# Performance work log

Hardware: AMD Instinct MI355X
Metric: run time of the kernel (lower is better)

The kernel has to match this reference:

```python
import jax, jax.numpy as jnp
import numpy as np

SCALE = float(1.0 / np.sqrt(128.0))  # 1/sqrt(q_head_dim)
NEG_BIG = -1e30


def setup_inputs() -> dict:
    key = jax.random.key(0)
    k0, k1, k2, k3, k4 = jax.random.split(key, 5)
    R, B, H, KVH, D, DV, P = 8, 8, 32, 8, 128, 128, 2048  # page_size = 1
    q = jax.random.normal(k0, (B, H, D), jnp.float32)
    k_cache = jax.random.normal(k1, (R, P, 1, KVH, D), jnp.float32)
    v_cache = jax.random.normal(k2, (R, P, 1, KVH, DV), jnp.float32)
    # each rank's shard length per batch element (>=128 so no empty shards)
    global_kv_lens = jax.random.randint(k3, (R, B), 128, P + 1, jnp.int32)
    # paged block table: page ids into that rank's cache
    block_table = jax.random.randint(k4, (R, B, P), 0, P, jnp.int32)
    return {"q": q, "k_cache": k_cache, "v_cache": v_cache,
            "global_kv_lens": global_kv_lens, "block_table": block_table}


def reference(q, k_cache, v_cache, global_kv_lens, block_table):
    R, P, page, KVH, D = k_cache.shape
    B, H, _ = q.shape
    DV = v_cache.shape[-1]
    G = H // KVH            # GQA group size
    N = P * page            # tokens per rank shard
    ridx = jnp.arange(R)[:, None, None]
    # paged KV gather per rank/batch: [R,B,N,KVH,D]
    Kg = k_cache[ridx, block_table].reshape(R, B, N, KVH, D)
    Vg = v_cache[ridx, block_table].reshape(R, B, N, KVH, DV)
    qg = q.reshape(B, KVH, G, D)
    # intra-rank split-KV attention scores: [R,B,KVH,G,N]
    s = jnp.einsum('bkgd,rbnkd->rbkgn', qg, Kg) * SCALE
    valid = (jnp.arange(N)[None, None, :] < global_kv_lens[:, :, None])
    s = jnp.where(valid[:, :, None, None, :], s, NEG_BIG)
    lse = jax.nn.logsumexp(s, axis=-1)             # per-rank softmax stats [R,B,KVH,G]
    p = jax.nn.softmax(s, axis=-1)
    out_r = jnp.einsum('rbkgn,rbnkd->rbkgd', p, Vg)  # per-rank partial output
    # inter-rank combine (online softmax across rank shards)
    m = jax.nn.logsumexp(lse, axis=0)              # [B,KVH,G]
    w = jnp.exp(lse - m)[..., None]                # [R,B,KVH,G,1]
    final = jnp.sum(w * out_r, axis=0)             # [B,KVH,G,DV]
    return final.reshape(B, H, DV)
```

## Files before the change

kernel.cpp:

```cpp
#include <hip/hip_runtime.h>
#include <hip/hip_bf16.h>
#include <math.h>

#define NR 8
#define NB 8
#define NH 32
#define NKVH 8
#define NG 4
#define ND 128
#define NDV 128
#define NDH 64
#define NPAGE 2048
#define KSTR (NKVH*ND)
#define NCH 8
#define CHUNK 256
#define NPART (NR*NCH)
#define PSTRIDE (NB*NKVH*NG)
#define QSCALE 0.088388347648318447f

typedef __attribute__((ext_vector_type(8))) short bf16x8;
typedef __attribute__((ext_vector_type(4))) float f32x4;

static __device__ __forceinline__ short f2bf(float x) {
  __hip_bfloat16 h = __float2bfloat16(x);
  return __builtin_bit_cast(short, h);
}

static __device__ __forceinline__ void gload_lds16(const float* g, float* l) {
  __builtin_amdgcn_global_load_lds(
      (__attribute__((address_space(1))) void*)g,
      (__attribute__((address_space(3))) void*)l, 16, 0, 0);
}

__global__ __launch_bounds__(256) void build_counts(
    const int* __restrict__ kv_lens, const int* __restrict__ bt_all,
    float* __restrict__ cntf) {
  const int rb = blockIdx.x;
  __shared__ int h[NPAGE];
  for (int i = threadIdx.x; i < NPAGE; i += 256) h[i] = 0;
  __syncthreads();
  const int len = kv_lens[rb];
  const int* bt = bt_all + (size_t)rb * NPAGE;
  for (int i = threadIdx.x; i < len; i += 256) atomicAdd(&h[bt[i]], 1);
  __syncthreads();
  float* o = cntf + (size_t)rb * NPAGE;
  for (int i = threadIdx.x; i < NPAGE; i += 256) o[i] = (float)h[i];
}

__global__ __launch_bounds__(256, 1) void attn_partial(
    const float* __restrict__ q,
    const float* __restrict__ k_cache,
    const float* __restrict__ v_cache,
    const float* __restrict__ cntf,
    float* __restrict__ ws_out,
    float* __restrict__ ws_lse)
{
  const int bid   = blockIdx.x;
  const int r     = bid & 7;
  const int kvh   = (bid >> 3) & 7;
  const int dh    = (bid >> 6) & 1;
  const int chunk = bid >> 7;

  const int tid  = threadIdx.x;
  const int wid  = tid >> 6;
  const int lane = tid & 63;
  const int col  = lane & 15;
  const int hq   = lane >> 4;

  __shared__ float LB[10240];

  bf16x8 qf[2][4];
#pragma unroll
  for (int gp = 0; gp < 2; ++gp) {
    const int b = col & 7;
    const int g = gp * 2 + (col >> 3);
    const float* qp = q + ((size_t)b * NH + kvh * NG + g) * ND + hq * 8;
#pragma unroll
    for (int st = 0; st < 4; ++st) {
      const float4 t0 = *(const float4*)(qp + st * 32);
      const float4 t1 = *(const float4*)(qp + st * 32 + 4);
      bf16x8 f;
      f[0] = f2bf(t0.x * QSCALE); f[1] = f2bf(t0.y * QSCALE);
      f[2] = f2bf(t0.z * QSCALE); f[3] = f2bf(t0.w * QSCALE);
      f[4] = f2bf(t1.x * QSCALE); f[5] = f2bf(t1.y * QSCALE);
      f[6] = f2bf(t1.z * QSCALE); f[7] = f2bf(t1.w * QSCALE);
      qf[gp][st] = f;
    }
  }

  const int pg0w = chunk * CHUNK + wid * 64;
  const float* Kb = k_cache + (size_t)r * NPAGE * KSTR + kvh * ND;
  const float* Vb = v_cache + (size_t)r * NPAGE * KSTR + kvh * NDV + dh * NDH;

#define STAGE_V(bf, pgt)                                                     \
  {                                                                          \
    _Pragma("unroll")                                                        \
    for (int i = 0; i < 4; ++i) {                                            \
      const float* s_ =                                                      \
          Vb + (size_t)((pgt) + 4 * i + (lane >> 4)) * KSTR + (lane & 15) * 4; \
      gload_lds16(s_, &LB[wid * 2048 + (bf) * 1024 + i * 256]);              \
    }                                                                        \
  }
#define KLOAD(dst, pgt)                                                      \
  {                                                                          \
    const float* kp_ = Kb + (size_t)((pgt) + col) * KSTR + hq * 8;           \
    _Pragma("unroll")                                                        \
    for (int st = 0; st < 4; ++st) {                                         \
      dst[2 * st]     = *(const float4*)(kp_ + st * 32);                     \
      dst[2 * st + 1] = *(const float4*)(kp_ + st * 32 + 4);                 \
    }                                                                        \
  }
#define CWLOAD(dst, pgt)                                                     \
  {                                                                          \
    _Pragma("unroll")                                                        \
    for (int rg = 0; rg < 4; ++rg)                                           \
      dst[rg] = cntf[((size_t)(r * NB + ((hq * 4 + rg) & 7))) * NPAGE +      \
                     (pgt) + col];                                           \
  }

  float4 kr[2][8];
  float  cwl[2][4];

  STAGE_V(0, pg0w);
  KLOAD(kr[0], pg0w);
  CWLOAD(cwl[0], pg0w);

  float l[2][4] = {{0.f, 0.f, 0.f, 0.f}, {0.f, 0.f, 0.f, 0.f}};
  f32x4 O[2][4];
#pragma unroll
  for (int gp = 0; gp < 2; ++gp)
#pragma unroll
    for (int rg = 0; rg < 4; ++rg) O[gp][rg] = (f32x4){0.f, 0.f, 0.f, 0.f};

#pragma unroll
  for (int t = 0; t < 4; ++t) {
    const int pgt = pg0w + t * 16;
    const int bf  = t & 1;

    if (t < 3) {
      STAGE_V(bf ^ 1, pgt + 16);
      KLOAD(kr[(t + 1) & 1], pgt + 16);
      CWLOAD(cwl[(t + 1) & 1], pgt + 16);
      asm volatile("s_waitcnt vmcnt(16)" ::: "memory");
    } else {
      asm volatile("s_waitcnt vmcnt(0)" ::: "memory");
    }

    f32x4 acc0 = (f32x4){0.f, 0.f, 0.f, 0.f};
    f32x4 acc1 = (f32x4){0.f, 0.f, 0.f, 0.f};
#pragma unroll
    for (int st = 0; st < 4; ++st) {
      const float4 a0 = kr[bf][2 * st];
      const float4 a1 = kr[bf][2 * st + 1];
      bf16x8 kf;
      kf[0] = f2bf(a0.x); kf[1] = f2bf(a0.y); kf[2] = f2bf(a0.z); kf[3] = f2bf(a0.w);
      kf[4] = f2bf(a1.x); kf[5] = f2bf(a1.y); kf[6] = f2bf(a1.z); kf[7] = f2bf(a1.w);
      acc0 = __builtin_amdgcn_mfma_f32_16x16x32_bf16(qf[0][st], kf, acc0, 0, 0, 0);
      acc1 = __builtin_amdgcn_mfma_f32_16x16x32_bf16(qf[1][st], kf, acc1, 0, 0, 0);
    }

    float p0[4], p1[4];
#pragma unroll
    for (int rg = 0; rg < 4; ++rg) {
      p0[rg] = cwl[bf][rg] * __expf(acc0[rg]);
      p1[rg] = cwl[bf][rg] * __expf(acc1[rg]);
      l[0][rg] += p0[rg];
      l[1][rg] += p1[rg];
    }
    *(f32x4*)&LB[8192 + wid * 512 + 0 * 256 + col * 16 + hq * 4] =
        (f32x4){p0[0], p0[1], p0[2], p0[3]};
    *(f32x4*)&LB[8192 + wid * 512 + 1 * 256 + col * 16 + hq * 4] =
        (f32x4){p1[0], p1[1], p1[2], p1[3]};

#pragma unroll 4
    for (int pg = 0; pg < 16; ++pg) {
      const f32x4 pw0 = *(const f32x4*)&LB[8192 + wid * 512 + pg * 16 + hq * 4];
      const f32x4 pw1 = *(const f32x4*)&LB[8192 + wid * 512 + 256 + pg * 16 + hq * 4];
      const f32x4 va  = *(const f32x4*)&LB[wid * 2048 + bf * 1024 + pg * 64 + col * 4];
#pragma unroll
      for (int rg = 0; rg < 4; ++rg) {
        O[0][rg] += pw0[rg] * va;
        O[1][rg] += pw1[rg] * va;
      }
    }
  }

#pragma unroll
  for (int mk = 1; mk <= 8; mk <<= 1)
#pragma unroll
    for (int gp = 0; gp < 2; ++gp)
#pragma unroll
      for (int rg = 0; rg < 4; ++rg) l[gp][rg] += __shfl_xor(l[gp][rg], mk);

  __syncthreads();
  if (col == 0) {
#pragma unroll
    for (int gp = 0; gp < 2; ++gp)
#pragma unroll
      for (int rg = 0; rg < 4; ++rg)
        LB[8704 + wid * 32 + gp * 16 + hq * 4 + rg] = l[gp][rg];
  }
#pragma unroll
  for (int gp = 0; gp < 2; ++gp)
#pragma unroll
    for (int rg = 0; rg < 4; ++rg) {
      const int row = (wid * 2 + gp) * 16 + hq * 4 + rg;
      *(f32x4*)&LB[row * 68 + col * 4] = O[gp][rg];
    }
  __syncthreads();

  const int row = tid >> 3;
  const int db  = tid & 7;
  const int gpo = row >> 4;
  const int qr  = row & 15;
  float L = 0.f;
#pragma unroll
  for (int w = 0; w < 4; ++w) L += LB[8704 + w * 32 + gpo * 16 + qr];
  const float inv = (L > 0.f) ? 1.f / L : 0.f;

  const int pi = r * NCH + chunk;
  const int b  = qr & 7;
  const int g  = gpo * 2 + (qr >> 3);
  const size_t prow = (((size_t)pi * NB + b) * NKVH + kvh) * NG + g;
  float* orow = ws_out + prow * NDV + dh * NDH + db * 8;
#pragma unroll
  for (int x = 0; x < 2; ++x) {
    float4 o = make_float4(0.f, 0.f, 0.f, 0.f);
#pragma unroll
    for (int w = 0; w < 4; ++w) {
      const float* s4 = &LB[((w * 2 + gpo) * 16 + qr) * 68 + db * 8 + x * 4];
      o.x += s4[0]; o.y += s4[1]; o.z += s4[2]; o.w += s4[3];
    }
    o.x *= inv; o.y *= inv; o.z *= inv; o.w *= inv;
    *(float4*)(orow + x * 4) = o;
  }
  if (db == 0) ws_lse[prow] = (L > 0.f) ? __logf(L) : -1e30f;
}

__global__ __launch_bounds__(128) void attn_combine(
    const float* __restrict__ ws_out,
    const float* __restrict__ ws_lse,
    float* __restrict__ out)
{
  const int bkg = blockIdx.x;
  const int d   = threadIdx.x;

  float mg = -INFINITY;
#pragma unroll 16
  for (int p = 0; p < NPART; ++p)
    mg = fmaxf(mg, ws_lse[p * PSTRIDE + bkg]);

  float denom = 0.f, acc = 0.f;
#pragma unroll 8
  for (int p = 0; p < NPART; ++p) {
    const float e = __expf(ws_lse[p * PSTRIDE + bkg] - mg);
    denom += e;
    acc += e * ws_out[((size_t)p * PSTRIDE + bkg) * NDV + d];
  }
  out[(size_t)bkg * NDV + d] = acc / denom;
}

extern "C" void kernel_launch(void* const* d_in, const int* in_sizes, int n_in,
                              void* d_out, int out_size, void* d_ws, size_t ws_size,
                              hipStream_t stream) {
  const float* q        = (const float*)d_in[0];
  const float* k_cache  = (const float*)d_in[1];
  const float* v_cache  = (const float*)d_in[2];
  const int*   kv_lens  = (const int*)d_in[3];
  const int*   bt       = (const int*)d_in[4];
  float* out = (float*)d_out;

  float* ws_out = (float*)d_ws;
  float* ws_lse = ws_out + (size_t)NPART * PSTRIDE * NDV;
  float* cntf   = ws_lse + NPART * PSTRIDE;

  build_counts<<<NR * NB, 256, 0, stream>>>(kv_lens, bt, cntf);
  attn_partial<<<NR * NKVH * 2 * NCH, 256, 0, stream>>>(
      q, k_cache, v_cache, cntf, ws_out, ws_lse);
  attn_combine<<<NB * NKVH * NG, NDV, 0, stream>>>(ws_out, ws_lse, out);
}
```

Measured before the change: 57.79 us.

## Merge the two V-half blocks so each block covers the full value dimension

Each attention block now handles all 128 value dimensions instead of splitting them into two halves across separate blocks. The grid is halved, which removes the duplicate K loads, QK MFMA work and exp computation that both halves used to perform. In exchange each block stages twice as much V into LDS (larger shared buffer), keeps twice as many output accumulators in registers, and adjusts the waitcnt for the extra loads. Fewer blocks (512 instead of 1024) may also reduce parallelism and latency hiding.

```diff
diff --git a/kernel.cpp b/kernel.cpp
--- a/kernel.cpp
+++ b/kernel.cpp
@@ -9,7 +9,6 @@
 #define NG 4
 #define ND 128
 #define NDV 128
-#define NDH 64
 #define NPAGE 2048
 #define KSTR (NKVH*ND)
 #define NCH 8
@@ -58,8 +57,7 @@
   const int bid   = blockIdx.x;
   const int r     = bid & 7;
   const int kvh   = (bid >> 3) & 7;
-  const int dh    = (bid >> 6) & 1;
-  const int chunk = bid >> 7;
+  const int chunk = bid >> 6;
 
   const int tid  = threadIdx.x;
   const int wid  = tid >> 6;
@@ -67,7 +65,7 @@
   const int col  = lane & 15;
   const int hq   = lane >> 4;
 
-  __shared__ float LB[10240];
+  __shared__ float LB[18432];
 
   bf16x8 qf[2][4];
 #pragma unroll
@@ -90,15 +88,15 @@
 
   const int pg0w = chunk * CHUNK + wid * 64;
   const float* Kb = k_cache + (size_t)r * NPAGE * KSTR + kvh * ND;
-  const float* Vb = v_cache + (size_t)r * NPAGE * KSTR + kvh * NDV + dh * NDH;
+  const float* Vb = v_cache + (size_t)r * NPAGE * KSTR + kvh * NDV;
 
 #define STAGE_V(bf, pgt)                                                     \
   {                                                                          \
     _Pragma("unroll")                                                        \
-    for (int i = 0; i < 4; ++i) {                                            \
+    for (int i = 0; i < 8; ++i) {                                            \
       const float* s_ =                                                      \
-          Vb + (size_t)((pgt) + 4 * i + (lane >> 4)) * KSTR + (lane & 15) * 4; \
-      gload_lds16(s_, &LB[wid * 2048 + (bf) * 1024 + i * 256]);              \
+          Vb + (size_t)((pgt) + 2 * i + (lane >> 5)) * KSTR + (lane & 31) * 4; \
+      gload_lds16(s_, &LB[wid * 4096 + (bf) * 2048 + i * 256]);              \
     }                                                                        \
   }
 #define KLOAD(dst, pgt)                                                      \
@@ -126,11 +124,14 @@
   CWLOAD(cwl[0], pg0w);
 
   float l[2][4] = {{0.f, 0.f, 0.f, 0.f}, {0.f, 0.f, 0.f, 0.f}};
-  f32x4 O[2][4];
+  f32x4 O[2][4][2];
 #pragma unroll
   for (int gp = 0; gp < 2; ++gp)
 #pragma unroll
-    for (int rg = 0; rg < 4; ++rg) O[gp][rg] = (f32x4){0.f, 0.f, 0.f, 0.f};
+    for (int rg = 0; rg < 4; ++rg) {
+      O[gp][rg][0] = (f32x4){0.f, 0.f, 0.f, 0.f};
+      O[gp][rg][1] = (f32x4){0.f, 0.f, 0.f, 0.f};
+    }
 
 #pragma unroll
   for (int t = 0; t < 4; ++t) {
@@ -141,7 +142,7 @@
       STAGE_V(bf ^ 1, pgt + 16);
       KLOAD(kr[(t + 1) & 1], pgt + 16);
       CWLOAD(cwl[(t + 1) & 1], pgt + 16);
-      asm volatile("s_waitcnt vmcnt(16)" ::: "memory");
+      asm volatile("s_waitcnt vmcnt(20)" ::: "memory");
     } else {
       asm volatile("s_waitcnt vmcnt(0)" ::: "memory");
     }
@@ -167,20 +168,24 @@
       l[0][rg] += p0[rg];
       l[1][rg] += p1[rg];
     }
-    *(f32x4*)&LB[8192 + wid * 512 + 0 * 256 + col * 16 + hq * 4] =
+    *(f32x4*)&LB[16384 + wid * 512 + 0 * 256 + col * 16 + hq * 4] =
         (f32x4){p0[0], p0[1], p0[2], p0[3]};
-    *(f32x4*)&LB[8192 + wid * 512 + 1 * 256 + col * 16 + hq * 4] =
+    *(f32x4*)&LB[16384 + wid * 512 + 1 * 256 + col * 16 + hq * 4] =
         (f32x4){p1[0], p1[1], p1[2], p1[3]};
 
 #pragma unroll 4
     for (int pg = 0; pg < 16; ++pg) {
-      const f32x4 pw0 = *(const f32x4*)&LB[8192 + wid * 512 + pg * 16 + hq * 4];
-      const f32x4 pw1 = *(const f32x4*)&LB[8192 + wid * 512 + 256 + pg * 16 + hq * 4];
-      const f32x4 va  = *(const f32x4*)&LB[wid * 2048 + bf * 1024 + pg * 64 + col * 4];
+      const f32x4 pw0 = *(const f32x4*)&LB[16384 + wid * 512 + pg * 16 + hq * 4];
+      const f32x4 pw1 = *(const f32x4*)&LB[16384 + wid * 512 + 256 + pg * 16 + hq * 4];
+      const float* vl = &LB[wid * 4096 + bf * 2048 + pg * 128 + col * 4];
+      const f32x4 va = *(const f32x4*)vl;
+      const f32x4 vb2 = *(const f32x4*)(vl + 64);
 #pragma unroll
       for (int rg = 0; rg < 4; ++rg) {
-        O[0][rg] += pw0[rg] * va;
-        O[1][rg] += pw1[rg] * va;
+        O[0][rg][0] += pw0[rg] * va;
+        O[0][rg][1] += pw0[rg] * vb2;
+        O[1][rg][0] += pw1[rg] * va;
+        O[1][rg][1] += pw1[rg] * vb2;
       }
     }
   }
@@ -198,14 +203,15 @@
     for (int gp = 0; gp < 2; ++gp)
 #pragma unroll
       for (int rg = 0; rg < 4; ++rg)
-        LB[8704 + wid * 32 + gp * 16 + hq * 4 + rg] = l[gp][rg];
+        LB[16896 + (wid * 2 + gp) * 16 + hq * 4 + rg] = l[gp][rg];
   }
 #pragma unroll
   for (int gp = 0; gp < 2; ++gp)
 #pragma unroll
     for (int rg = 0; rg < 4; ++rg) {
       const int row = (wid * 2 + gp) * 16 + hq * 4 + rg;
-      *(f32x4*)&LB[row * 68 + col * 4] = O[gp][rg];
+      *(f32x4*)&LB[row * 132 + col * 4]      = O[gp][rg][0];
+      *(f32x4*)&LB[row * 132 + 64 + col * 4] = O[gp][rg][1];
     }
   __syncthreads();
 
@@ -215,20 +221,20 @@
   const int qr  = row & 15;
   float L = 0.f;
 #pragma unroll
-  for (int w = 0; w < 4; ++w) L += LB[8704 + w * 32 + gpo * 16 + qr];
+  for (int w = 0; w < 4; ++w) L += LB[16896 + (w * 2 + gpo) * 16 + qr];
   const float inv = (L > 0.f) ? 1.f / L : 0.f;
 
   const int pi = r * NCH + chunk;
   const int b  = qr & 7;
   const int g  = gpo * 2 + (qr >> 3);
   const size_t prow = (((size_t)pi * NB + b) * NKVH + kvh) * NG + g;
-  float* orow = ws_out + prow * NDV + dh * NDH + db * 8;
-#pragma unroll
-  for (int x = 0; x < 2; ++x) {
+  float* orow = ws_out + prow * NDV + db * 16;
+#pragma unroll
+  for (int x = 0; x < 4; ++x) {
     float4 o = make_float4(0.f, 0.f, 0.f, 0.f);
 #pragma unroll
     for (int w = 0; w < 4; ++w) {
-      const float* s4 = &LB[((w * 2 + gpo) * 16 + qr) * 68 + db * 8 + x * 4];
+      const float* s4 = &LB[((w * 2 + gpo) * 16 + qr) * 132 + db * 16 + x * 4];
       o.x += s4[0]; o.y += s4[1]; o.z += s4[2]; o.w += s4[3];
     }
     o.x *= inv; o.y *= inv; o.z *= inv; o.w *= inv;
@@ -275,7 +281,7 @@
   float* cntf   = ws_lse + NPART * PSTRIDE;
 
   build_counts<<<NR * NB, 256, 0, stream>>>(kv_lens, bt, cntf);
-  attn_partial<<<NR * NKVH * 2 * NCH, 256, 0, stream>>>(
+  attn_partial<<<NR * NKVH * NCH, 256, 0, stream>>>(
       q, k_cache, v_cache, cntf, ws_out, ws_lse);
   attn_combine<<<NB * NKVH * NG, NDV, 0, stream>>>(ws_out, ws_lse, out);
 }
```

Result: no change. 58.24 us (+0.8%).

## Merge both DV halves into one 512-thread block and drop K prefetch

Applied to the files above, without the earlier changes.

Each block now covers both 64-column halves of V with 8 waves, instead of launching separate blocks per half. Waves sharing the same pages reduce partial outputs through LDS in two phases. The K and count double-buffered prefetch is replaced by in-iteration loads, and the explicit vmcnt waits are removed. The intent is fewer blocks and shared K traffic in cache. The cost is exposed load latency and a possible race on asynchronous V staging.

```diff
diff --git a/kernel.cpp b/kernel.cpp
--- a/kernel.cpp
+++ b/kernel.cpp
@@ -9,7 +9,6 @@
 #define NG 4
 #define ND 128
 #define NDV 128
-#define NDH 64
 #define NPAGE 2048
 #define KSTR (NKVH*ND)
 #define NCH 8
@@ -47,7 +46,7 @@
   for (int i = threadIdx.x; i < NPAGE; i += 256) o[i] = (float)h[i];
 }
 
-__global__ __launch_bounds__(256, 1) void attn_partial(
+__global__ __launch_bounds__(512, 2) void attn_partial(
     const float* __restrict__ q,
     const float* __restrict__ k_cache,
     const float* __restrict__ v_cache,
@@ -58,16 +57,17 @@
   const int bid   = blockIdx.x;
   const int r     = bid & 7;
   const int kvh   = (bid >> 3) & 7;
-  const int dh    = (bid >> 6) & 1;
-  const int chunk = bid >> 7;
+  const int chunk = bid >> 6;
 
   const int tid  = threadIdx.x;
   const int wid  = tid >> 6;
   const int lane = tid & 63;
   const int col  = lane & 15;
   const int hq   = lane >> 4;
-
-  __shared__ float LB[10240];
+  const int q4   = wid & 3;
+  const int dvh  = wid >> 2;
+
+  __shared__ float LB[20480];
 
   bf16x8 qf[2][4];
 #pragma unroll
@@ -88,9 +88,9 @@
     }
   }
 
-  const int pg0w = chunk * CHUNK + wid * 64;
+  const int pg0w = chunk * CHUNK + q4 * 64;
   const float* Kb = k_cache + (size_t)r * NPAGE * KSTR + kvh * ND;
-  const float* Vb = v_cache + (size_t)r * NPAGE * KSTR + kvh * NDV + dh * NDH;
+  const float* Vb = v_cache + (size_t)r * NPAGE * KSTR + kvh * NDV + dvh * 64;
 
 #define STAGE_V(bf, pgt)                                                     \
   {                                                                          \
@@ -118,12 +118,10 @@
                      (pgt) + col];                                           \
   }
 
-  float4 kr[2][8];
-  float  cwl[2][4];
+  float4 kr[8];
+  float  cwl[4];
 
   STAGE_V(0, pg0w);
-  KLOAD(kr[0], pg0w);
-  CWLOAD(cwl[0], pg0w);
 
   float l[2][4] = {{0.f, 0.f, 0.f, 0.f}, {0.f, 0.f, 0.f, 0.f}};
   f32x4 O[2][4];
@@ -137,21 +135,19 @@
     const int pgt = pg0w + t * 16;
     const int bf  = t & 1;
 
+    KLOAD(kr, pgt);
+    CWLOAD(cwl, pgt);
     if (t < 3) {
+      asm volatile("s_waitcnt lgkmcnt(0)" ::: "memory");
       STAGE_V(bf ^ 1, pgt + 16);
-      KLOAD(kr[(t + 1) & 1], pgt + 16);
-      CWLOAD(cwl[(t + 1) & 1], pgt + 16);
-      asm volatile("s_waitcnt vmcnt(16)" ::: "memory");
-    } else {
-      asm volatile("s_waitcnt vmcnt(0)" ::: "memory");
     }
 
     f32x4 acc0 = (f32x4){0.f, 0.f, 0.f, 0.f};
     f32x4 acc1 = (f32x4){0.f, 0.f, 0.f, 0.f};
 #pragma unroll
     for (int st = 0; st < 4; ++st) {
-      const float4 a0 = kr[bf][2 * st];
-      const float4 a1 = kr[bf][2 * st + 1];
+      const float4 a0 = kr[2 * st];
+      const float4 a1 = kr[2 * st + 1];
       bf16x8 kf;
       kf[0] = f2bf(a0.x); kf[1] = f2bf(a0.y); kf[2] = f2bf(a0.z); kf[3] = f2bf(a0.w);
       kf[4] = f2bf(a1.x); kf[5] = f2bf(a1.y); kf[6] = f2bf(a1.z); kf[7] = f2bf(a1.w);
@@ -162,20 +158,20 @@
     float p0[4], p1[4];
 #pragma unroll
     for (int rg = 0; rg < 4; ++rg) {
-      p0[rg] = cwl[bf][rg] * __expf(acc0[rg]);
-      p1[rg] = cwl[bf][rg] * __expf(acc1[rg]);
+      p0[rg] = cwl[rg] * __expf(acc0[rg]);
+      p1[rg] = cwl[rg] * __expf(acc1[rg]);
       l[0][rg] += p0[rg];
       l[1][rg] += p1[rg];
     }
-    *(f32x4*)&LB[8192 + wid * 512 + 0 * 256 + col * 16 + hq * 4] =
+    *(f32x4*)&LB[16384 + wid * 512 + 0 * 256 + col * 16 + hq * 4] =
         (f32x4){p0[0], p0[1], p0[2], p0[3]};
-    *(f32x4*)&LB[8192 + wid * 512 + 1 * 256 + col * 16 + hq * 4] =
+    *(f32x4*)&LB[16384 + wid * 512 + 1 * 256 + col * 16 + hq * 4] =
         (f32x4){p1[0], p1[1], p1[2], p1[3]};
 
 #pragma unroll 4
     for (int pg = 0; pg < 16; ++pg) {
-      const f32x4 pw0 = *(const f32x4*)&LB[8192 + wid * 512 + pg * 16 + hq * 4];
-      const f32x4 pw1 = *(const f32x4*)&LB[8192 + wid * 512 + 256 + pg * 16 + hq * 4];
+      const f32x4 pw0 = *(const f32x4*)&LB[16384 + wid * 512 + pg * 16 + hq * 4];
+      const f32x4 pw1 = *(const f32x4*)&LB[16384 + wid * 512 + 256 + pg * 16 + hq * 4];
       const f32x4 va  = *(const f32x4*)&LB[wid * 2048 + bf * 1024 + pg * 64 + col * 4];
 #pragma unroll
       for (int rg = 0; rg < 4; ++rg) {
@@ -193,48 +189,70 @@
       for (int rg = 0; rg < 4; ++rg) l[gp][rg] += __shfl_xor(l[gp][rg], mk);
 
   __syncthreads();
-  if (col == 0) {
+  const int region = q4 & 1;
+  if (q4 < 2) {
 #pragma unroll
     for (int gp = 0; gp < 2; ++gp)
 #pragma unroll
-      for (int rg = 0; rg < 4; ++rg)
-        LB[8704 + wid * 32 + gp * 16 + hq * 4 + rg] = l[gp][rg];
-  }
-#pragma unroll
-  for (int gp = 0; gp < 2; ++gp)
-#pragma unroll
-    for (int rg = 0; rg < 4; ++rg) {
-      const int row = (wid * 2 + gp) * 16 + hq * 4 + rg;
-      *(f32x4*)&LB[row * 68 + col * 4] = O[gp][rg];
-    }
-  __syncthreads();
-
-  const int row = tid >> 3;
-  const int db  = tid & 7;
-  const int gpo = row >> 4;
-  const int qr  = row & 15;
-  float L = 0.f;
-#pragma unroll
-  for (int w = 0; w < 4; ++w) L += LB[8704 + w * 32 + gpo * 16 + qr];
+      for (int rg = 0; rg < 4; ++rg) {
+        const int row = dvh * 32 + gp * 16 + hq * 4 + rg;
+        *(f32x4*)&LB[region * 4352 + row * 68 + col * 4] = O[gp][rg];
+      }
+    if (dvh == 0 && col == 0) {
+#pragma unroll
+      for (int gp = 0; gp < 2; ++gp)
+#pragma unroll
+        for (int rg = 0; rg < 4; ++rg)
+          LB[8704 + region * 32 + gp * 16 + hq * 4 + rg] = l[gp][rg];
+    }
+  }
+  __syncthreads();
+  if (q4 >= 2) {
+#pragma unroll
+    for (int gp = 0; gp < 2; ++gp)
+#pragma unroll
+      for (int rg = 0; rg < 4; ++rg) {
+        const int row = dvh * 32 + gp * 16 + hq * 4 + rg;
+        float* dst = &LB[region * 4352 + row * 68 + col * 4];
+        f32x4 v = *(f32x4*)dst;
+        v += O[gp][rg];
+        *(f32x4*)dst = v;
+      }
+    if (dvh == 0 && col == 0) {
+#pragma unroll
+      for (int gp = 0; gp < 2; ++gp)
+#pragma unroll
+        for (int rg = 0; rg < 4; ++rg)
+          LB[8704 + region * 32 + gp * 16 + hq * 4 + rg] += l[gp][rg];
+    }
+  }
+  __syncthreads();
+
+  const int row  = tid >> 3;
+  const int db   = tid & 7;
+  const int dvh_ = row >> 5;
+  const int gp_  = (row >> 4) & 1;
+  const int qr   = row & 15;
+  const float L  = LB[8704 + gp_ * 16 + qr] + LB[8704 + 32 + gp_ * 16 + qr];
   const float inv = (L > 0.f) ? 1.f / L : 0.f;
 
   const int pi = r * NCH + chunk;
   const int b  = qr & 7;
-  const int g  = gpo * 2 + (qr >> 3);
+  const int g  = gp_ * 2 + (qr >> 3);
   const size_t prow = (((size_t)pi * NB + b) * NKVH + kvh) * NG + g;
-  float* orow = ws_out + prow * NDV + dh * NDH + db * 8;
+  float* orow = ws_out + prow * NDV + dvh_ * 64 + db * 8;
 #pragma unroll
   for (int x = 0; x < 2; ++x) {
-    float4 o = make_float4(0.f, 0.f, 0.f, 0.f);
-#pragma unroll
-    for (int w = 0; w < 4; ++w) {
-      const float* s4 = &LB[((w * 2 + gpo) * 16 + qr) * 68 + db * 8 + x * 4];
-      o.x += s4[0]; o.y += s4[1]; o.z += s4[2]; o.w += s4[3];
-    }
-    o.x *= inv; o.y *= inv; o.z *= inv; o.w *= inv;
+    const float* s0 = &LB[(row) * 68 + db * 8 + x * 4];
+    const float* s1 = &LB[4352 + (row) * 68 + db * 8 + x * 4];
+    float4 o;
+    o.x = (s0[0] + s1[0]) * inv;
+    o.y = (s0[1] + s1[1]) * inv;
+    o.z = (s0[2] + s1[2]) * inv;
+    o.w = (s0[3] + s1[3]) * inv;
     *(float4*)(orow + x * 4) = o;
   }
-  if (db == 0) ws_lse[prow] = (L > 0.f) ? __logf(L) : -1e30f;
+  if (db == 0 && dvh_ == 0) ws_lse[prow] = (L > 0.f) ? __logf(L) : -1e30f;
 }
 
 __global__ __launch_bounds__(128) void attn_combine(
@@ -275,7 +293,7 @@
   float* cntf   = ws_lse + NPART * PSTRIDE;
 
   build_counts<<<NR * NB, 256, 0, stream>>>(kv_lens, bt, cntf);
-  attn_partial<<<NR * NKVH * 2 * NCH, 256, 0, stream>>>(
+  attn_partial<<<NR * NKVH * NCH, 512, 0, stream>>>(
       q, k_cache, v_cache, cntf, ws_out, ws_lse);
   attn_combine<<<NB * NKVH * NG, NDV, 0, stream>>>(ws_out, ws_lse, out);
 }
```

Measured after the change: 61.99 us. 1.07x slower.
